# Optimization experiments

Measured on AMD Instinct MI355X. Metric: run time of the kernel, lower is better.

## Reference

```python
import jax, jax.numpy as jnp
import numpy as np

N, C, T, V = 32, 64, 256, 25
IC, NS = 16, 3  # inter_channels = C // 4, num_subset = 3
EPS = 1e-5


def _bn(x, g, b, m, v):
    # inference-mode BatchNorm2d over channel dim of [N, C, T, V]
    scale = g / jnp.sqrt(v + EPS)
    return (x - m[:, None, None]) * scale[:, None, None] + b[:, None, None]


def _conv1x1(x, w, b):
    # 1x1 Conv2d on [N, C, T, V]; w: [O, C], b: [O]
    return jnp.einsum('nctv,oc->notv', x, w) + b[None, :, None, None]


def setup_inputs() -> dict:
    key = jax.random.key(0)
    ks = iter(jax.random.split(key, 40))
    def nrm(shape, s=0.05):
        return jax.random.normal(next(ks), shape, jnp.float32) * s
    inp = {}
    inp['feature'] = jax.random.normal(next(ks), (N, C, T, V), jnp.float32)
    inp['hidden'] = jax.random.normal(next(ks), (N, C, T, V), jnp.float32)
    inp['A'] = jax.random.uniform(next(ks), (NS, V, V), jnp.float32) * 0.1
    inp['PA'] = jnp.full((NS, V, V), 1e-6, jnp.float32)
    inp['conv_a_w'] = nrm((NS, IC, C)); inp['conv_a_b'] = nrm((NS, IC))
    inp['conv_b_w'] = nrm((NS, IC, C)); inp['conv_b_b'] = nrm((NS, IC))
    inp['conv_d_w'] = nrm((NS, C, C));  inp['conv_d_b'] = nrm((NS, C))
    inp['gbn_g'] = 0.5 + jax.random.uniform(next(ks), (C,), jnp.float32)
    inp['gbn_b'] = nrm((C,))
    inp['gbn_m'] = nrm((C,))
    inp['gbn_v'] = 0.5 + jax.random.uniform(next(ks), (C,), jnp.float32)
    inp['tcn_w'] = nrm((C, C, 9, 1)); inp['tcn_b'] = nrm((C,))
    inp['tbn_g'] = 0.5 + jax.random.uniform(next(ks), (C,), jnp.float32)
    inp['tbn_b'] = nrm((C,))
    inp['tbn_m'] = nrm((C,))
    inp['tbn_v'] = 0.5 + jax.random.uniform(next(ks), (C,), jnp.float32)
    for nme in ['W_ir', 'W_ii', 'W_in', 'W_hr', 'W_hi', 'W_hh']:
        inp[nme] = nrm((C, C))
    for nme in ['b_ir', 'b_ii', 'b_in']:
        inp[nme] = nrm((C,))
    return inp


def _tcn_gcn(h, A, PA, caw, cab, cbw, cbb, cdw, cdb,
             gbn_g, gbn_b, gbn_m, gbn_v, tcn_w, tcn_b,
             tbn_g, tbn_b, tbn_m, tbn_v):
    # unit_gcn (in == out -> down is identity)
    Aeff = A + PA  # [NS, V, V]
    scale = 1.0 / (IC * T)
    y = 0.0
    h_flat = h.reshape(N, C * T, V)
    for i in range(NS):
        a = _conv1x1(h, caw[i], cab[i])            # [N, IC, T, V]
        b = _conv1x1(h, cbw[i], cbb[i])            # [N, IC, T, V]
        A1 = a.transpose(0, 3, 1, 2).reshape(N, V, IC * T)
        A2 = b.reshape(N, IC * T, V)
        att = jax.nn.softmax(jnp.einsum('nvk,nkw->nvw', A1, A2) * scale, axis=-2)
        att = att + Aeff[i]                         # [N, V, V]
        z = jnp.einsum('nkv,nvw->nkw', h_flat, att).reshape(N, C, T, V)
        y = y + _conv1x1(z, cdw[i], cdb[i])
    gcn_out = jax.nn.relu(_bn(y, gbn_g, gbn_b, gbn_m, gbn_v) + h)
    # unit_tcn: (9,1) conv, pad (4,0), stride 1
    t = jax.lax.conv_general_dilated(
        gcn_out, tcn_w, window_strides=(1, 1), padding=[(4, 4), (0, 0)],
        dimension_numbers=('NCHW', 'OIHW', 'NCHW'))
    t = t + tcn_b[None, :, None, None]
    t = _bn(t, tbn_g, tbn_b, tbn_m, tbn_v)
    # residual is identity (in==out, stride 1)
    return jax.nn.relu(t + h)


def reference(feature, hidden, A, PA, conv_a_w, conv_a_b, conv_b_w, conv_b_b,
              conv_d_w, conv_d_b, gbn_g, gbn_b, gbn_m, gbn_v, tcn_w, tcn_b,
              tbn_g, tbn_b, tbn_m, tbn_v, W_ir, b_ir, W_ii, b_ii, W_in, b_in,
              W_hr, W_hi, W_hh):
    msg = _tcn_gcn(hidden, A, PA, conv_a_w, conv_a_b, conv_b_w, conv_b_b,
                   conv_d_w, conv_d_b, gbn_g, gbn_b, gbn_m, gbn_v,
                   tcn_w, tcn_b, tbn_g, tbn_b, tbn_m, tbn_v)
    feat = feature.transpose(0, 2, 3, 1).reshape(N, T * V, C)
    msg2 = msg.transpose(0, 2, 3, 1).reshape(N, T * V, C)
    hid2 = hidden.transpose(0, 2, 3, 1).reshape(N, T * V, C)
    r = jax.nn.sigmoid(feat @ W_ir.T + b_ir + msg2 @ W_hr.T)
    z = jax.nn.sigmoid(feat @ W_ii.T + b_ii + msg2 @ W_hi.T)
    n = jnp.tanh(feat @ W_in.T + b_in + r * (msg2 @ W_hh.T))
    h_new = (1.0 - z) * n + z * hid2
    return h_new.reshape(N, T, V, C).transpose(0, 3, 1, 2)
```

## Files before the change

### kernel.cpp

```cpp
#include <hip/hip_runtime.h>
#include <math.h>

#define TV 6400
#define NTOT 32

typedef __attribute__((ext_vector_type(8))) short short8;
typedef __attribute__((ext_vector_type(4))) short short4v;
typedef __attribute__((ext_vector_type(4))) float f32x4;

__device__ __forceinline__ float b2f(short s) {
  unsigned u = ((unsigned)(unsigned short)s) << 16;
  return __uint_as_float(u);
}
__device__ __forceinline__ short f2b(float f) {
  unsigned u = __float_as_uint(f);
  u = (u + 0x7FFF + ((u >> 16) & 1)) >> 16;
  return (short)u;
}

__global__ __launch_bounds__(256) void pack_kernel(
    const float* __restrict__ tcn_w, const float* __restrict__ caw,
    const float* __restrict__ cbw, const float* __restrict__ cdw,
    const float* __restrict__ W_ir, const float* __restrict__ W_ii,
    const float* __restrict__ W_in, const float* __restrict__ W_hr,
    const float* __restrict__ W_hi, const float* __restrict__ W_hh,
    const float* __restrict__ cab, const float* __restrict__ cbb,
    const float* __restrict__ b_ir, const float* __restrict__ b_ii,
    const float* __restrict__ b_in,
    short* __restrict__ P, float* __restrict__ Pb)
{
  int idx = blockIdx.x * 256 + threadIdx.x;
  if (idx < 9984) {
    int lane = idx & 63;
    int rest = idx >> 6;
    int c = rest & 1;
    rest >>= 1;
    int mloc = lane & 15, kb = c * 32 + (lane >> 4) * 8;
    short8 v;
    if (rest < 6) {
      int m = rest * 16 + mloc;
      for (int i = 0; i < 8; ++i)
        v[i] = f2b(m < 48 ? caw[m * 64 + kb + i] : cbw[(m - 48) * 64 + kb + i]);
    } else if (rest < 18) {
      int m = (rest - 6) * 16 + mloc;
      for (int i = 0; i < 8; ++i) v[i] = f2b(cdw[m * 64 + kb + i]);
    } else if (rest < 30) {
      int m = (rest - 18) * 16 + mloc;
      const float* W = (m < 64) ? W_ir : (m < 128 ? W_ii : W_in);
      int mr = m & 63;
      for (int i = 0; i < 8; ++i) v[i] = f2b(W[mr * 64 + kb + i]);
    } else if (rest < 42) {
      int m = (rest - 30) * 16 + mloc;
      const float* W = (m < 64) ? W_hr : (m < 128 ? W_hi : W_hh);
      int mr = m & 63;
      for (int i = 0; i < 8; ++i) v[i] = f2b(W[mr * 64 + kb + i]);
    } else {
      int t = rest - 42;
      int kk = t >> 2, mf = t & 3;
      int o = mf * 16 + mloc;
      for (int i = 0; i < 8; ++i) v[i] = f2b(tcn_w[o * 576 + (kb + i) * 9 + kk]);
    }
    *(short8*)(P + (size_t)idx * 8) = v;
  } else if (idx < 9984 + 288) {
    int r = idx - 9984;
    if (r < 96) Pb[r] = (r < 48) ? cab[r] : cbb[r - 48];
    else {
      int q = r - 96;
      Pb[r] = (q < 64) ? b_ir[q] : (q < 128 ? b_ii[q - 64] : b_in[q - 128]);
    }
  }
}

__global__ __launch_bounds__(256) void convert_kernel(
    const float* __restrict__ hid, const float* __restrict__ feat,
    short* __restrict__ hidK, short* __restrict__ featK)
{
  int j = blockIdx.x * 256 + threadIdx.x;
  int gy = blockIdx.y;
  int n = blockIdx.z;
  const float* src = ((gy < 8) ? hid : feat) + ((long)n * 64 + (long)(gy & 7) * 8) * TV + j;
  short* dst = ((gy < 8) ? hidK : featK) + (((long)n * 8 + (gy & 7)) * TV + j) * 8;
  short8 o;
#pragma unroll
  for (int i = 0; i < 8; ++i) o[i] = f2b(src[(long)i * TV]);
  *(short8*)dst = o;
}

__global__ __launch_bounds__(256) void ab_gemm(
    const short8* __restrict__ Wp, const short8* __restrict__ Bk,
    short* __restrict__ Cout, const float* __restrict__ bias)
{
  const int tid = threadIdx.x;
  const int lane = tid & 63, w = tid >> 6;
  const int q = lane >> 4, lj = lane & 15;
  const int j0 = blockIdx.x * 128;
  const int n = blockIdx.y;
  const short8* Bn = Bk + (long)n * 8 * TV;
  short* Cn = Cout + (long)n * 96 * TV;

  f32x4 acc[6][2];
  for (int a = 0; a < 6; ++a) for (int b = 0; b < 2; ++b)
    acc[a][b] = (f32x4){0.f, 0.f, 0.f, 0.f};

  for (int c = 0; c < 2; ++c) {
    short8 bf0 = Bn[(long)(c * 4 + q) * TV + j0 + (w * 2 + 0) * 16 + lj];
    short8 bf1 = Bn[(long)(c * 4 + q) * TV + j0 + (w * 2 + 1) * 16 + lj];
#pragma unroll
    for (int mf = 0; mf < 6; ++mf) {
      short8 af = Wp[(mf * 2 + c) * 64 + lane];
      acc[mf][0] = __builtin_amdgcn_mfma_f32_16x16x32_bf16(af, bf0, acc[mf][0], 0, 0, 0);
      acc[mf][1] = __builtin_amdgcn_mfma_f32_16x16x32_bf16(af, bf1, acc[mf][1], 0, 0, 0);
    }
  }
#pragma unroll
  for (int mf = 0; mf < 6; ++mf) {
    int k0 = mf * 16 + q * 4;
    int g = k0 >> 3, i0 = k0 & 7;
    float bv[4];
#pragma unroll
    for (int r = 0; r < 4; ++r) bv[r] = bias[k0 + r];
#pragma unroll
    for (int jf = 0; jf < 2; ++jf) {
      int j = j0 + (w * 2 + jf) * 16 + lj;
      short4v o4;
#pragma unroll
      for (int r = 0; r < 4; ++r) o4[r] = f2b(acc[mf][jf][r] + bv[r]);
      *(short4v*)(Cn + ((long)g * TV + j) * 8 + i0) = o4;
    }
  }
}

__global__ __launch_bounds__(256) void att_partial(
    const short* __restrict__ abK, float* __restrict__ partial)
{
  const int ch = blockIdx.x, i = blockIdx.y, n = blockIdx.z;
  __shared__ float sA[6400], sB[6400];
  const int tid = threadIdx.x;
  const long nb = (long)n * 96 * TV;
  const int t0 = ch * 16;
  for (int idx = tid; idx < 800; idx += 256) {
    int gh = idx / 400, jl = idx - gh * 400;
    long j = (long)t0 * 25 + jl;
    short8 va = *(const short8*)&abK[nb + ((long)(2 * i + gh) * TV + j) * 8];
    short8 vb = *(const short8*)&abK[nb + ((long)(6 + 2 * i + gh) * TV + j) * 8];
#pragma unroll
    for (int e = 0; e < 8; ++e) {
      sA[(gh * 8 + e) * 400 + jl] = b2f(va[e]);
      sB[(gh * 8 + e) * 400 + jl] = b2f(vb[e]);
    }
  }
  __syncthreads();
  const int a0 = tid >> 4, b0 = tid & 15;
  const int v1 = a0 + 16, w1 = b0 + 16;
  const int v1c = (v1 < 25) ? v1 : 0, w1c = (w1 < 25) ? w1 : 0;
  float acc00 = 0, acc01 = 0, acc10 = 0, acc11 = 0;
#pragma unroll 8
  for (int r = 0; r < 256; ++r) {
    float av0 = sA[r * 25 + a0], av1 = sA[r * 25 + v1c];
    float bw0 = sB[r * 25 + b0], bw1 = sB[r * 25 + w1c];
    acc00 += av0 * bw0; acc01 += av0 * bw1;
    acc10 += av1 * bw0; acc11 += av1 * bw1;
  }
  const float scale = 1.0f / 4096.0f;
  float* pp = partial + (((long)(n * 3 + i) * 16) + ch) * 625;
  pp[a0 * 25 + b0] = acc00 * scale;
  if (w1 < 25) pp[a0 * 25 + w1] = acc01 * scale;
  if (v1 < 25) pp[v1 * 25 + b0] = acc10 * scale;
  if (v1 < 25 && w1 < 25) pp[v1 * 25 + w1] = acc11 * scale;
}

__global__ __launch_bounds__(256) void att_reduce(
    const float* __restrict__ partial, const float* __restrict__ Amat,
    const float* __restrict__ PAmat, short* __restrict__ attP)
{
  const int i = blockIdx.x, n = blockIdx.y;
  __shared__ float sL[625];
  const int tid = threadIdx.x;
  const float* pp = partial + ((long)(n * 3 + i) * 16) * 625;
  for (int idx = tid; idx < 625; idx += 256) {
    float s = 0.f;
#pragma unroll
    for (int c = 0; c < 16; ++c) s += pp[c * 625 + idx];
    sL[idx] = s;
  }
  __syncthreads();
  if (tid < 25) {
    const int w = tid;
    float mx = -1e30f;
#pragma unroll
    for (int v = 0; v < 25; ++v) mx = fmaxf(mx, sL[v * 25 + w]);
    float e[25];
    float s = 0.f;
#pragma unroll
    for (int v = 0; v < 25; ++v) { e[v] = __expf(sL[v * 25 + w] - mx); s += e[v]; }
    float inv = 1.f / s;
#pragma unroll
    for (int v = 0; v < 25; ++v)
      sL[v * 25 + w] = e[v] * inv + Amat[i * 625 + v * 25 + w] + PAmat[i * 625 + v * 25 + w];
  }
  __syncthreads();
  if (tid < 128) {
    int wf = tid >> 6, lane = tid & 63;
    int q = lane >> 4, lj = lane & 15;
    int w = wf * 16 + lj;
    short8 o = {0, 0, 0, 0, 0, 0, 0, 0};
    if (w < 25) {
#pragma unroll
      for (int e2 = 0; e2 < 8; ++e2) {
        int v = q * 8 + e2;
        if (v < 25) o[e2] = f2b(sL[v * 25 + w]);
      }
    }
    *(short8*)(attP + (size_t)(((long)(n * 3 + i) * 2 + wf) * 64 + lane) * 8) = o;
  }
}

#define UST 114
#define OST 101
__global__ __launch_bounds__(256) void gcn_fused(
    const short8* __restrict__ Wu, const short8* __restrict__ attP,
    const short8* __restrict__ hidK, const float* __restrict__ cdb,
    const float* __restrict__ gg, const float* __restrict__ gb,
    const float* __restrict__ gm, const float* __restrict__ gv,
    short* __restrict__ gcnK)
{
  __shared__ short uT[192 * UST];
  __shared__ short sOut[64 * OST];
  __shared__ float A2[64], B2[64];
  const int tid = threadIdx.x;
  if (tid < 64) {
    float sc = gg[tid] * rsqrtf(gv[tid] + 1e-5f);
    A2[tid] = sc;
    float bias = cdb[tid] + cdb[64 + tid] + cdb[128 + tid];
    B2[tid] = bias * sc + (gb[tid] - gm[tid] * sc);
  }
  const int lane = tid & 63, w = tid >> 6;
  const int q = lane >> 4, lj = lane & 15;
  const int tt = blockIdx.x, n = blockIdx.y;
  const int jb = tt * 100;
  const short8* Hn = hidK + (long)n * 8 * TV;

  f32x4 uacc[3][7];
  for (int a = 0; a < 3; ++a) for (int b = 0; b < 7; ++b)
    uacc[a][b] = (f32x4){0.f, 0.f, 0.f, 0.f};
  for (int c = 0; c < 2; ++c) {
    short8 bf[7];
#pragma unroll
    for (int jf = 0; jf < 7; ++jf)
      bf[jf] = Hn[(long)(c * 4 + q) * TV + jb + jf * 16 + lj];
#pragma unroll
    for (int ml = 0; ml < 3; ++ml) {
      short8 af = Wu[((w * 3 + ml) * 2 + c) * 64 + lane];
#pragma unroll
      for (int jf = 0; jf < 7; ++jf)
        uacc[ml][jf] = __builtin_amdgcn_mfma_f32_16x16x32_bf16(af, bf[jf], uacc[ml][jf], 0, 0, 0);
    }
  }
#pragma unroll
  for (int ml = 0; ml < 3; ++ml) {
    int row0 = (w * 3 + ml) * 16 + q * 4;
#pragma unroll
    for (int jf = 0; jf < 7; ++jf) {
      int col = jf * 16 + lj;
#pragma unroll
      for (int r = 0; r < 4; ++r)
        uT[(row0 + r) * UST + col] = f2b(uacc[ml][jf][r]);
    }
  }
  __syncthreads();

  const int colt = w * 25;
  short8 attA[6];
#pragma unroll
  for (int i = 0; i < 3; ++i)
#pragma unroll
    for (int wf = 0; wf < 2; ++wf)
      attA[i * 2 + wf] = attP[((long)(n * 3 + i) * 2 + wf) * 64 + lane];

  f32x4 macc[2][4];
  for (int a = 0; a < 2; ++a) for (int b = 0; b < 4; ++b)
    macc[a][b] = (f32x4){0.f, 0.f, 0.f, 0.f};
#pragma unroll
  for (int i = 0; i < 3; ++i) {
#pragma unroll
    for (int of = 0; of < 4; ++of) {
      int row = i * 64 + of * 16 + lj;
      short8 bf;
#pragma unroll
      for (int e = 0; e < 8; ++e)
        bf[e] = uT[row * UST + colt + q * 8 + e];
      macc[0][of] = __builtin_amdgcn_mfma_f32_16x16x32_bf16(attA[i * 2 + 0], bf, macc[0][of], 0, 0, 0);
      macc[1][of] = __builtin_amdgcn_mfma_f32_16x16x32_bf16(attA[i * 2 + 1], bf, macc[1][of], 0, 0, 0);
    }
  }
#pragma unroll
  for (int wf = 0; wf < 2; ++wf)
#pragma unroll
    for (int of = 0; of < 4; ++of)
#pragma unroll
      for (int r = 0; r < 4; ++r) {
        int wl = wf * 16 + q * 4 + r;
        if (wl < 25)
          sOut[(of * 16 + lj) * OST + colt + wl] = f2b(macc[wf][of][r]);
      }
  __syncthreads();

  const short* HnS = (const short*)Hn;
  short* Gn = gcnK + (long)n * 64 * TV;
  for (int u2 = tid; u2 < 800; u2 += 256) {
    int col = u2 % 100, og = u2 / 100;
    long ubase = ((long)og * TV + jb + col) * 8;
    short8 h8 = *(const short8*)&HnS[ubase];
    short8 o8;
#pragma unroll
    for (int e = 0; e < 8; ++e) {
      int o = og * 8 + e;
      float acc = b2f(sOut[o * OST + col]);
      float vv = fmaxf(acc * A2[o] + B2[o] + b2f(h8[e]), 0.f);
      o8[e] = f2b(vv);
    }
    *(short8*)&Gn[ubase] = o8;
  }
}

__global__ __launch_bounds__(256) void tcn_mfma(
    const short8* __restrict__ wTp, const short8* __restrict__ gcnK,
    const short* __restrict__ hidK, const float* __restrict__ tcn_b,
    const float* __restrict__ pbg, const float* __restrict__ pbb,
    const float* __restrict__ pbm, const float* __restrict__ pbv,
    short* __restrict__ msgK)
{
  __shared__ float A2[64], B2[64];
  const int tid = threadIdx.x;
  if (tid < 64) {
    float sc = pbg[tid] * rsqrtf(pbv[tid] + 1e-5f);
    A2[tid] = sc;
    B2[tid] = tcn_b[tid] * sc + (pbb[tid] - pbm[tid] * sc);
  }
  __syncthreads();
  const int lane = tid & 63, w = tid >> 6;
  const int q = lane >> 4, lj = lane & 15;
  const int j0 = blockIdx.x * 128;
  const int n = blockIdx.y;
  const short8* Bn = gcnK + (long)n * 8 * TV;
  const short8 zero8 = {0, 0, 0, 0, 0, 0, 0, 0};

  f32x4 acc[4][2];
  for (int a = 0; a < 4; ++a) for (int b = 0; b < 2; ++b)
    acc[a][b] = (f32x4){0.f, 0.f, 0.f, 0.f};

  for (int kk = 0; kk < 9; ++kk) {
    const int shift = (kk - 4) * 25;
    for (int c = 0; c < 2; ++c) {
      short8 bfv[2];
#pragma unroll
      for (int jf = 0; jf < 2; ++jf) {
        int col = j0 + (w * 2 + jf) * 16 + lj + shift;
        bool valid = ((unsigned)col < (unsigned)TV);
        short8 t = Bn[(long)(c * 4 + q) * TV + (valid ? col : 0)];
        bfv[jf] = valid ? t : zero8;
      }
#pragma unroll
      for (int mf = 0; mf < 4; ++mf) {
        short8 af = wTp[((kk * 4 + mf) * 2 + c) * 64 + lane];
        acc[mf][0] = __builtin_amdgcn_mfma_f32_16x16x32_bf16(af, bfv[0], acc[mf][0], 0, 0, 0);
        acc[mf][1] = __builtin_amdgcn_mfma_f32_16x16x32_bf16(af, bfv[1], acc[mf][1], 0, 0, 0);
      }
    }
  }

  short* Mn = msgK + (long)n * 64 * TV;
  const short* Hn = hidK + (long)n * 64 * TV;
#pragma unroll
  for (int mf = 0; mf < 4; ++mf) {
    int k0 = mf * 16 + q * 4;
    int g = k0 >> 3, i0 = k0 & 7;
#pragma unroll
    for (int jf = 0; jf < 2; ++jf) {
      int j = j0 + (w * 2 + jf) * 16 + lj;
      long base = ((long)g * TV + j) * 8 + i0;
      short4v h4 = *(const short4v*)&Hn[base];
      short4v o4;
#pragma unroll
      for (int r = 0; r < 4; ++r) {
        float v = acc[mf][jf][r] * A2[k0 + r] + B2[k0 + r] + b2f(h4[r]);
        o4[r] = f2b(fmaxf(v, 0.f));
      }
      *(short4v*)&Mn[base] = o4;
    }
  }
}

__global__ __launch_bounds__(256) void gru_mfma(
    const short8* __restrict__ WFp, const short8* __restrict__ WHp,
    const float* __restrict__ bF, const short8* __restrict__ featK,
    const short8* __restrict__ msgK, const short* __restrict__ hidK,
    float* __restrict__ outp)
{
  __shared__ __align__(16) char smem[49152];
  __shared__ float sBias[192];
  short8* sW = (short8*)smem;
  float* sOut = (float*)smem;
  const int tid = threadIdx.x;
  for (int idx = tid; idx < 1536; idx += 256) {
    sW[idx] = WFp[idx];
    sW[1536 + idx] = WHp[idx];
  }
  if (tid < 192) sBias[tid] = bF[tid];
  __syncthreads();

  const int lane = tid & 63, w = tid >> 6;
  const int q = lane >> 4, lj = lane & 15;
  const int j0 = blockIdx.x * 64;
  const int n = blockIdx.y;
  const int j = j0 + w * 16 + lj;
  const short8* Fn = featK + (long)n * 8 * TV;
  const short8* Mn = msgK + (long)n * 8 * TV;

  f32x4 accF[12], accH[12];
  for (int a = 0; a < 12; ++a) {
    accF[a] = (f32x4){0.f, 0.f, 0.f, 0.f};
    accH[a] = (f32x4){0.f, 0.f, 0.f, 0.f};
  }
  for (int c = 0; c < 2; ++c) {
    short8 bFf = Fn[(long)(c * 4 + q) * TV + j];
    short8 bHf = Mn[(long)(c * 4 + q) * TV + j];
#pragma unroll
    for (int mf = 0; mf < 12; ++mf) {
      short8 af = sW[(mf * 2 + c) * 64 + lane];
      accF[mf] = __builtin_amdgcn_mfma_f32_16x16x32_bf16(af, bFf, accF[mf], 0, 0, 0);
      short8 ah = sW[1536 + (mf * 2 + c) * 64 + lane];
      accH[mf] = __builtin_amdgcn_mfma_f32_16x16x32_bf16(ah, bHf, accH[mf], 0, 0, 0);
    }
  }
  __syncthreads();

  const short* Hn = hidK + (long)n * 64 * TV;
#pragma unroll
  for (int mf = 0; mf < 4; ++mf) {
    int k0 = mf * 16 + q * 4;
    int g = k0 >> 3, i0 = k0 & 7;
    short4v h4 = *(const short4v*)&Hn[((long)g * TV + j) * 8 + i0];
#pragma unroll
    for (int r = 0; r < 4; ++r) {
      int o = k0 + r;
      float rp = accF[mf][r] + sBias[o] + accH[mf][r];
      float zp = accF[mf + 4][r] + sBias[64 + o] + accH[mf + 4][r];
      float np = accF[mf + 8][r] + sBias[128 + o];
      float rv = 1.f / (1.f + __expf(-rp));
      float zv = 1.f / (1.f + __expf(-zp));
      float nn = tanhf(np + rv * accH[mf + 8][r]);
      float hv = b2f(h4[r]);
      sOut[o * 68 + (w * 16 + lj)] = (1.f - zv) * nn + zv * hv;
    }
  }
  __syncthreads();
  float* On = outp + (long)n * 64 * TV;
  for (int u2 = tid; u2 < 1024; u2 += 256) {
    int row = u2 >> 4, c4 = u2 & 15;
    float4 vv = *(const float4*)&sOut[row * 68 + c4 * 4];
    *(float4*)&On[(long)row * TV + j0 + c4 * 4] = vv;
  }
}

extern "C" void kernel_launch(void* const* d_in, const int* in_sizes, int n_in,
                              void* d_out, int out_size, void* d_ws, size_t ws_size,
                              hipStream_t stream)
{
  const float* feature = (const float*)d_in[0];
  const float* hidden  = (const float*)d_in[1];
  const float* Amat    = (const float*)d_in[2];
  const float* PAmat   = (const float*)d_in[3];
  const float* caw = (const float*)d_in[4];
  const float* cab = (const float*)d_in[5];
  const float* cbw = (const float*)d_in[6];
  const float* cbb = (const float*)d_in[7];
  const float* cdw = (const float*)d_in[8];
  const float* cdb = (const float*)d_in[9];
  const float* gbn_g = (const float*)d_in[10];
  const float* gbn_b = (const float*)d_in[11];
  const float* gbn_m = (const float*)d_in[12];
  const float* gbn_v = (const float*)d_in[13];
  const float* tcn_w = (const float*)d_in[14];
  const float* tcn_b = (const float*)d_in[15];
  const float* tbn_g = (const float*)d_in[16];
  const float* tbn_b = (const float*)d_in[17];
  const float* tbn_m = (const float*)d_in[18];
  const float* tbn_v = (const float*)d_in[19];
  const float* W_ir = (const float*)d_in[20];
  const float* W_ii = (const float*)d_in[21];
  const float* W_in = (const float*)d_in[22];
  const float* W_hr = (const float*)d_in[23];
  const float* W_hi = (const float*)d_in[24];
  const float* W_hh = (const float*)d_in[25];
  const float* b_ir = (const float*)d_in[26];
  const float* b_ii = (const float*)d_in[27];
  const float* b_in = (const float*)d_in[28];
  float* out = (float*)d_out;

  int Nc = NTOT;
  while (Nc > 1) {
    size_t need = (size_t)352 * TV * 2 * Nc + (size_t)Nc * 30000 * 4 +
                  (size_t)Nc * 3072 * 2 + 79872 * 2 + 288 * 4 + 4096;
    if (need <= ws_size) break;
    Nc >>= 1;
  }

  char* p = (char*)d_ws;
  short* hidK = (short*)p;  p += (size_t)Nc * 64 * TV * 2;
  short* featK = (short*)p; p += (size_t)Nc * 64 * TV * 2;
  short* abK = (short*)p;   p += (size_t)Nc * 96 * TV * 2;
  short* gcnK = (short*)p;  p += (size_t)Nc * 64 * TV * 2;
  short* msgK = (short*)p;  p += (size_t)Nc * 64 * TV * 2;
  float* partial = (float*)p; p += (size_t)Nc * 30000 * 4;
  short* attP = (short*)p;    p += (size_t)Nc * 3072 * 2;
  p = (char*)(((size_t)p + 15) & ~(size_t)15);
  short* P = (short*)p;       p += 79872 * 2;
  float* Pb = (float*)p;

  pack_kernel<<<dim3(41), dim3(256), 0, stream>>>(
      tcn_w, caw, cbw, cdw, W_ir, W_ii, W_in, W_hr, W_hi, W_hh,
      cab, cbb, b_ir, b_ii, b_in, P, Pb);

  const long s64 = (long)64 * TV;
  for (int c0 = 0; c0 < NTOT; c0 += Nc) {
    const float* hidc = hidden + (long)c0 * s64;
    const float* featc = feature + (long)c0 * s64;
    float* outc = out + (long)c0 * s64;

    convert_kernel<<<dim3(25, 16, Nc), 256, 0, stream>>>(hidc, featc, hidK, featK);
    ab_gemm<<<dim3(50, Nc), 256, 0, stream>>>(
        (const short8*)P, (const short8*)hidK, abK, Pb);
    att_partial<<<dim3(16, 3, Nc), 256, 0, stream>>>(abK, partial);
    att_reduce<<<dim3(3, Nc), 256, 0, stream>>>(partial, Amat, PAmat, attP);
    gcn_fused<<<dim3(64, Nc), 256, 0, stream>>>(
        (const short8*)P + 768, (const short8*)attP, (const short8*)hidK,
        cdb, gbn_g, gbn_b, gbn_m, gbn_v, gcnK);
    tcn_mfma<<<dim3(50, Nc), 256, 0, stream>>>(
        (const short8*)P + 5376, (const short8*)gcnK, hidK, tcn_b,
        tbn_g, tbn_b, tbn_m, tbn_v, msgK);
    gru_mfma<<<dim3(100, Nc), 256, 0, stream>>>(
        (const short8*)P + 2304, (const short8*)P + 3840, Pb + 96,
        (const short8*)featK, (const short8*)msgK, hidK, outc);
  }
}
```

Before: 366.6 us.

## Fuse temporal conv into GRU kernel and pad GCN smem for vector loads

Merges the TCN convolution kernel into the GRU kernel, so the message tensor stays in shared memory and is never written to or read back from global memory. This removes one launch and a full bf16 intermediate round trip, at the cost of smaller column tiles per block. The GCN shared buffer is re-laid out so each 25-column group is padded to 32 with zeros, which lets the B operand be loaded with one 16-byte read instead of eight scalar ones. Sigmoid and tanh are replaced with exp plus hardware-reciprocal approximations, which lowers precision slightly.

New measurement: 389.7 us. 1.06x slower.

```diff
diff --git a/kernel.cpp b/kernel.cpp
--- a/kernel.cpp
+++ b/kernel.cpp
@@ -16,6 +16,14 @@
   unsigned u = __float_as_uint(f);
   u = (u + 0x7FFF + ((u >> 16) & 1)) >> 16;
   return (short)u;
+}
+__device__ __forceinline__ float fsig(float x) {
+  return __builtin_amdgcn_rcpf(1.f + __expf(-x));
+}
+__device__ __forceinline__ float ftanh(float x) {
+  float x2 = fminf(fmaxf(2.f * x, -80.f), 80.f);
+  float t = __expf(x2);
+  return (t - 1.f) * __builtin_amdgcn_rcpf(t + 1.f);
 }
 
 __global__ __launch_bounds__(256) void pack_kernel(
@@ -215,7 +223,7 @@
   }
 }
 
-#define UST 114
+#define UST 136
 #define OST 101
 __global__ __launch_bounds__(256) void gcn_fused(
     const short8* __restrict__ Wu, const short8* __restrict__ attP,
@@ -224,7 +232,7 @@
     const float* __restrict__ gm, const float* __restrict__ gv,
     short* __restrict__ gcnK)
 {
-  __shared__ short uT[192 * UST];
+  __shared__ __align__(16) short uT[192 * UST];
   __shared__ short sOut[64 * OST];
   __shared__ float A2[64], B2[64];
   const int tid = threadIdx.x;
@@ -234,6 +242,11 @@
     float bias = cdb[tid] + cdb[64 + tid] + cdb[128 + tid];
     B2[tid] = bias * sc + (gb[tid] - gm[tid] * sc);
   }
+  for (int idx = tid; idx < 5376; idx += 256) {
+    int row = idx / 28, rr = idx - row * 28;
+    int g = rr / 7, s = 25 + (rr - g * 7);
+    uT[row * UST + g * 32 + s] = 0;
+  }
   const int lane = tid & 63, w = tid >> 6;
   const int q = lane >> 4, lj = lane & 15;
   const int tt = blockIdx.x, n = blockIdx.y;
@@ -262,9 +275,12 @@
 #pragma unroll
     for (int jf = 0; jf < 7; ++jf) {
       int col = jf * 16 + lj;
-#pragma unroll
-      for (int r = 0; r < 4; ++r)
-        uT[(row0 + r) * UST + col] = f2b(uacc[ml][jf][r]);
+      if (col < 100) {
+        int cc = (col / 25) * 32 + (col % 25);
+#pragma unroll
+        for (int r = 0; r < 4; ++r)
+          uT[(row0 + r) * UST + cc] = f2b(uacc[ml][jf][r]);
+      }
     }
   }
   __syncthreads();
@@ -285,10 +301,7 @@
 #pragma unroll
     for (int of = 0; of < 4; ++of) {
       int row = i * 64 + of * 16 + lj;
-      short8 bf;
-#pragma unroll
-      for (int e = 0; e < 8; ++e)
-        bf[e] = uT[row * UST + colt + q * 8 + e];
+      short8 bf = *(const short8*)&uT[row * UST + w * 32 + q * 8];
       macc[0][of] = __builtin_amdgcn_mfma_f32_16x16x32_bf16(attA[i * 2 + 0], bf, macc[0][of], 0, 0, 0);
       macc[1][of] = __builtin_amdgcn_mfma_f32_16x16x32_bf16(attA[i * 2 + 1], bf, macc[1][of], 0, 0, 0);
     }
@@ -323,82 +336,19 @@
   }
 }
 
-__global__ __launch_bounds__(256) void tcn_mfma(
+__global__ __launch_bounds__(256) void tcn_gru_fused(
     const short8* __restrict__ wTp, const short8* __restrict__ gcnK,
     const short* __restrict__ hidK, const float* __restrict__ tcn_b,
-    const float* __restrict__ pbg, const float* __restrict__ pbb,
-    const float* __restrict__ pbm, const float* __restrict__ pbv,
-    short* __restrict__ msgK)
-{
-  __shared__ float A2[64], B2[64];
-  const int tid = threadIdx.x;
-  if (tid < 64) {
-    float sc = pbg[tid] * rsqrtf(pbv[tid] + 1e-5f);
-    A2[tid] = sc;
-    B2[tid] = tcn_b[tid] * sc + (pbb[tid] - pbm[tid] * sc);
-  }
-  __syncthreads();
-  const int lane = tid & 63, w = tid >> 6;
-  const int q = lane >> 4, lj = lane & 15;
-  const int j0 = blockIdx.x * 128;
-  const int n = blockIdx.y;
-  const short8* Bn = gcnK + (long)n * 8 * TV;
-  const short8 zero8 = {0, 0, 0, 0, 0, 0, 0, 0};
-
-  f32x4 acc[4][2];
-  for (int a = 0; a < 4; ++a) for (int b = 0; b < 2; ++b)
-    acc[a][b] = (f32x4){0.f, 0.f, 0.f, 0.f};
-
-  for (int kk = 0; kk < 9; ++kk) {
-    const int shift = (kk - 4) * 25;
-    for (int c = 0; c < 2; ++c) {
-      short8 bfv[2];
-#pragma unroll
-      for (int jf = 0; jf < 2; ++jf) {
-        int col = j0 + (w * 2 + jf) * 16 + lj + shift;
-        bool valid = ((unsigned)col < (unsigned)TV);
-        short8 t = Bn[(long)(c * 4 + q) * TV + (valid ? col : 0)];
-        bfv[jf] = valid ? t : zero8;
-      }
-#pragma unroll
-      for (int mf = 0; mf < 4; ++mf) {
-        short8 af = wTp[((kk * 4 + mf) * 2 + c) * 64 + lane];
-        acc[mf][0] = __builtin_amdgcn_mfma_f32_16x16x32_bf16(af, bfv[0], acc[mf][0], 0, 0, 0);
-        acc[mf][1] = __builtin_amdgcn_mfma_f32_16x16x32_bf16(af, bfv[1], acc[mf][1], 0, 0, 0);
-      }
-    }
-  }
-
-  short* Mn = msgK + (long)n * 64 * TV;
-  const short* Hn = hidK + (long)n * 64 * TV;
-#pragma unroll
-  for (int mf = 0; mf < 4; ++mf) {
-    int k0 = mf * 16 + q * 4;
-    int g = k0 >> 3, i0 = k0 & 7;
-#pragma unroll
-    for (int jf = 0; jf < 2; ++jf) {
-      int j = j0 + (w * 2 + jf) * 16 + lj;
-      long base = ((long)g * TV + j) * 8 + i0;
-      short4v h4 = *(const short4v*)&Hn[base];
-      short4v o4;
-#pragma unroll
-      for (int r = 0; r < 4; ++r) {
-        float v = acc[mf][jf][r] * A2[k0 + r] + B2[k0 + r] + b2f(h4[r]);
-        o4[r] = f2b(fmaxf(v, 0.f));
-      }
-      *(short4v*)&Mn[base] = o4;
-    }
-  }
-}
-
-__global__ __launch_bounds__(256) void gru_mfma(
+    const float* __restrict__ tg, const float* __restrict__ tb2,
+    const float* __restrict__ tm, const float* __restrict__ tvv,
     const short8* __restrict__ WFp, const short8* __restrict__ WHp,
     const float* __restrict__ bF, const short8* __restrict__ featK,
-    const short8* __restrict__ msgK, const short* __restrict__ hidK,
     float* __restrict__ outp)
 {
   __shared__ __align__(16) char smem[49152];
+  __shared__ __align__(16) short sMsg[4096];
   __shared__ float sBias[192];
+  __shared__ float A2[64], B2[64];
   short8* sW = (short8*)smem;
   float* sOut = (float*)smem;
   const int tid = threadIdx.x;
@@ -407,24 +357,62 @@
     sW[1536 + idx] = WHp[idx];
   }
   if (tid < 192) sBias[tid] = bF[tid];
+  if (tid < 64) {
+    float sc = tg[tid] * rsqrtf(tvv[tid] + 1e-5f);
+    A2[tid] = sc;
+    B2[tid] = tcn_b[tid] * sc + (tb2[tid] - tm[tid] * sc);
+  }
   __syncthreads();
 
   const int lane = tid & 63, w = tid >> 6;
   const int q = lane >> 4, lj = lane & 15;
-  const int j0 = blockIdx.x * 64;
-  const int n = blockIdx.y;
-  const int j = j0 + w * 16 + lj;
-  const short8* Fn = featK + (long)n * 8 * TV;
-  const short8* Mn = msgK + (long)n * 8 * TV;
+  const int j0 = blockIdx.x * 64, n = blockIdx.y;
+  const int jcol = j0 + w * 16 + lj;
+  const int cloc = w * 16 + lj;
+  const short8* Bn = gcnK + (long)n * 8 * TV;
+  const short8 zero8 = {0, 0, 0, 0, 0, 0, 0, 0};
+
+  f32x4 acc[4];
+  for (int a = 0; a < 4; ++a) acc[a] = (f32x4){0.f, 0.f, 0.f, 0.f};
+  for (int kk = 0; kk < 9; ++kk) {
+    const int shift = (kk - 4) * 25;
+    for (int c = 0; c < 2; ++c) {
+      int col = jcol + shift;
+      bool valid = ((unsigned)col < (unsigned)TV);
+      short8 t = Bn[(long)(c * 4 + q) * TV + (valid ? col : 0)];
+      short8 bf = valid ? t : zero8;
+#pragma unroll
+      for (int mf = 0; mf < 4; ++mf) {
+        short8 af = wTp[((kk * 4 + mf) * 2 + c) * 64 + lane];
+        acc[mf] = __builtin_amdgcn_mfma_f32_16x16x32_bf16(af, bf, acc[mf], 0, 0, 0);
+      }
+    }
+  }
+  const short* HnS = hidK + (long)n * 64 * TV;
+#pragma unroll
+  for (int mf = 0; mf < 4; ++mf) {
+    int k0 = mf * 16 + q * 4;
+    int g = k0 >> 3, i0 = k0 & 7;
+    short4v h4 = *(const short4v*)&HnS[((long)g * TV + jcol) * 8 + i0];
+    short4v o4;
+#pragma unroll
+    for (int r = 0; r < 4; ++r) {
+      float v = acc[mf][r] * A2[k0 + r] + B2[k0 + r] + b2f(h4[r]);
+      o4[r] = f2b(fmaxf(v, 0.f));
+    }
+    *(short4v*)&sMsg[(g * 64 + cloc) * 8 + i0] = o4;
+  }
+  __syncthreads();
 
   f32x4 accF[12], accH[12];
   for (int a = 0; a < 12; ++a) {
     accF[a] = (f32x4){0.f, 0.f, 0.f, 0.f};
     accH[a] = (f32x4){0.f, 0.f, 0.f, 0.f};
   }
+  const short8* Fn = featK + (long)n * 8 * TV;
   for (int c = 0; c < 2; ++c) {
-    short8 bFf = Fn[(long)(c * 4 + q) * TV + j];
-    short8 bHf = Mn[(long)(c * 4 + q) * TV + j];
+    short8 bFf = Fn[(long)(c * 4 + q) * TV + jcol];
+    short8 bHf = *(const short8*)&sMsg[((c * 4 + q) * 64 + cloc) * 8];
 #pragma unroll
     for (int mf = 0; mf < 12; ++mf) {
       short8 af = sW[(mf * 2 + c) * 64 + lane];
@@ -435,23 +423,22 @@
   }
   __syncthreads();
 
-  const short* Hn = hidK + (long)n * 64 * TV;
 #pragma unroll
   for (int mf = 0; mf < 4; ++mf) {
     int k0 = mf * 16 + q * 4;
     int g = k0 >> 3, i0 = k0 & 7;
-    short4v h4 = *(const short4v*)&Hn[((long)g * TV + j) * 8 + i0];
+    short4v h4 = *(const short4v*)&HnS[((long)g * TV + jcol) * 8 + i0];
 #pragma unroll
     for (int r = 0; r < 4; ++r) {
       int o = k0 + r;
       float rp = accF[mf][r] + sBias[o] + accH[mf][r];
       float zp = accF[mf + 4][r] + sBias[64 + o] + accH[mf + 4][r];
       float np = accF[mf + 8][r] + sBias[128 + o];
-      float rv = 1.f / (1.f + __expf(-rp));
-      float zv = 1.f / (1.f + __expf(-zp));
-      float nn = tanhf(np + rv * accH[mf + 8][r]);
+      float rv = fsig(rp);
+      float zv = fsig(zp);
+      float nn = ftanh(np + rv * accH[mf + 8][r]);
       float hv = b2f(h4[r]);
-      sOut[o * 68 + (w * 16 + lj)] = (1.f - zv) * nn + zv * hv;
+      sOut[o * 68 + cloc] = (1.f - zv) * nn + zv * hv;
     }
   }
   __syncthreads();
@@ -500,7 +487,7 @@
 
   int Nc = NTOT;
   while (Nc > 1) {
-    size_t need = (size_t)352 * TV * 2 * Nc + (size_t)Nc * 30000 * 4 +
+    size_t need = (size_t)288 * TV * 2 * Nc + (size_t)Nc * 30000 * 4 +
                   (size_t)Nc * 3072 * 2 + 79872 * 2 + 288 * 4 + 4096;
     if (need <= ws_size) break;
     Nc >>= 1;
@@ -511,7 +498,6 @@
   short* featK = (short*)p; p += (size_t)Nc * 64 * TV * 2;
   short* abK = (short*)p;   p += (size_t)Nc * 96 * TV * 2;
   short* gcnK = (short*)p;  p += (size_t)Nc * 64 * TV * 2;
-  short* msgK = (short*)p;  p += (size_t)Nc * 64 * TV * 2;
   float* partial = (float*)p; p += (size_t)Nc * 30000 * 4;
   short* attP = (short*)p;    p += (size_t)Nc * 3072 * 2;
   p = (char*)(((size_t)p + 15) & ~(size_t)15);
@@ -536,11 +522,10 @@
     gcn_fused<<<dim3(64, Nc), 256, 0, stream>>>(
         (const short8*)P + 768, (const short8*)attP, (const short8*)hidK,
         cdb, gbn_g, gbn_b, gbn_m, gbn_v, gcnK);
-    tcn_mfma<<<dim3(50, Nc), 256, 0, stream>>>(
+    tcn_gru_fused<<<dim3(100, Nc), 256, 0, stream>>>(
         (const short8*)P + 5376, (const short8*)gcnK, hidK, tcn_b,
-        tbn_g, tbn_b, tbn_m, tbn_v, msgK);
-    gru_mfma<<<dim3(100, Nc), 256, 0, stream>>>(
+        tbn_g, tbn_b, tbn_m, tbn_v,
         (const short8*)P + 2304, (const short8*)P + 3840, Pb + 96,
-        (const short8*)featK, (const short8*)msgK, hidK, outc);
-  }
-}
+        (const short8*)featK, outc);
+  }
+}
```
